# Kernel optimization log

Hardware: AMD Instinct MI355X
Metric: run time of the kernel (lower is better)

## Reference

```python
import jax, jax.numpy as jnp
import numpy as np

DIM = 768
HEADS = 12
HD = DIM // HEADS  # 64
EPS = 1e-5


def _ln(t, g, b):
    # LayerNorm over last axis (head_dim), torch eps=1e-5, biased variance
    mu = jnp.mean(t, axis=-1, keepdims=True)
    var = jnp.mean(jnp.square(t - mu), axis=-1, keepdims=True)
    return (t - mu) * jax.lax.rsqrt(var + EPS) * g + b


def _get_qkv(t, W, bias, gq, bq, gk, bk):
    bs, n, c = t.shape
    qkv = t @ W.T + bias                      # [bs, n, 3c]
    q, k, v = jnp.split(qkv, 3, axis=-1)
    def heads(u):
        return u.reshape(bs, n, HEADS, HD).transpose(0, 2, 1, 3)  # [bs,H,n,hd]
    q, k, v = heads(q), heads(k), heads(v)
    return _ln(q, gq, bq), _ln(k, gk, bk), v


def setup_inputs() -> dict:
    key = jax.random.key(0)
    ks = jax.random.split(key, 12)
    s_in = 1.0 / np.sqrt(DIM)
    d = {
        "x": jax.random.normal(ks[0], (4, 1024, DIM), jnp.float32),
        "y": jax.random.normal(ks[1], (4, 1024, DIM), jnp.float32),
        "Wqkv_x": jax.random.uniform(ks[2], (3 * DIM, DIM), jnp.float32, -s_in, s_in),
        "bqkv_x": jnp.zeros((3 * DIM,), jnp.float32),
        "Wqkv_y": jax.random.uniform(ks[3], (3 * DIM, DIM), jnp.float32, -s_in, s_in),
        "bqkv_y": jnp.zeros((3 * DIM,), jnp.float32),
        "Wproj_x": jax.random.uniform(ks[4], (DIM, DIM), jnp.float32, -s_in, s_in),
        "bproj_x": jnp.zeros((DIM,), jnp.float32),
        "Wproj_y": jax.random.uniform(ks[5], (DIM, DIM), jnp.float32, -s_in, s_in),
        "bproj_y": jnp.zeros((DIM,), jnp.float32),
        "gq_x": jnp.ones((HD,), jnp.float32), "bq_x": jnp.zeros((HD,), jnp.float32),
        "gk_x": jnp.ones((HD,), jnp.float32), "bk_x": jnp.zeros((HD,), jnp.float32),
        "gq_y": jnp.ones((HD,), jnp.float32), "bq_y": jnp.zeros((HD,), jnp.float32),
        "gk_y": jnp.ones((HD,), jnp.float32), "bk_y": jnp.zeros((HD,), jnp.float32),
    }
    return d


def reference(x, y, Wqkv_x, bqkv_x, Wqkv_y, bqkv_y, Wproj_x, bproj_x,
              Wproj_y, bproj_y, gq_x, bq_x, gk_x, bk_x, gq_y, bq_y, gk_y, bk_y):
    bs, n, c = x.shape
    qx, kx, vx = _get_qkv(x, Wqkv_x, bqkv_x, gq_x, bq_x, gk_x, bk_x)
    qy, ky, vy = _get_qkv(y, Wqkv_y, bqkv_y, gq_y, bq_y, gk_y, bk_y)
    q = jnp.concatenate([qx, qy], axis=2)     # [bs,H,n+m,hd]
    k = jnp.concatenate([kx, ky], axis=2)
    v = jnp.concatenate([vx, vy], axis=2)
    score = jnp.einsum("bhqd,bhkd->bhqk", q, k) / np.sqrt(HD)
    attn = jax.nn.softmax(score, axis=-1)
    out = jnp.einsum("bhqk,bhkd->bhqd", attn, v)  # [bs,H,n+m,hd]
    out = out.transpose(0, 2, 1, 3).reshape(bs, -1, c)
    ox, oy = out[:, :n, :], out[:, n:, :]
    return ox @ Wproj_x.T + bproj_x, oy @ Wproj_y.T + bproj_y
```

## Files before the change

### kernel.cpp

```cpp
#include <hip/hip_runtime.h>
#include <stdint.h>

typedef unsigned int u32;
typedef __attribute__((ext_vector_type(8))) __bf16 bf16x8;
typedef __attribute__((ext_vector_type(8))) short s16x8;
typedef __attribute__((ext_vector_type(4))) short s16x4;
typedef __attribute__((ext_vector_type(4))) float f32x4;


__device__ __forceinline__ short f2bf(float f) {
    __bf16 h = (__bf16)f;
    return __builtin_bit_cast(short, h);
}

__device__ __forceinline__ bf16x8 asbf(s16x8 v) {
    return __builtin_bit_cast(bf16x8, v);
}

__device__ __forceinline__ void gl_lds16(const void* g, void* l) {
    __builtin_amdgcn_global_load_lds((__attribute__((address_space(1))) u32*)g,
                                     (__attribute__((address_space(3))) u32*)l,
                                     16, 0, 0);
}



__global__ __launch_bounds__(256) void pack_tiles(
    const float* __restrict__ x,  short* __restrict__ xP,
    const float* __restrict__ y,  short* __restrict__ yP,
    const float* __restrict__ wqx, short* __restrict__ wqxP,
    const float* __restrict__ wqy, short* __restrict__ wqyP,
    const float* __restrict__ wpx, short* __restrict__ wpxP,
    const float* __restrict__ wpy, short* __restrict__ wpyP)
{
    const int tid  = threadIdx.x;
    const int w    = tid >> 6, lane = tid & 63;
    const int lam  = lane & 15, quad = lane >> 4;

    int t = blockIdx.x;
    const float* src; short* dst;
    if (t < 384)                 { src = x;   dst = xP; }
    else if ((t -= 384) < 384)   { src = y;   dst = yP; }
    else if ((t -= 384) < 216)   { src = wqx; dst = wqxP; }
    else if ((t -= 216) < 216)   { src = wqy; dst = wqyP; }
    else if ((t -= 216) < 72)    { src = wpx; dst = wpxP; }
    else                         { t -= 72;  src = wpy; dst = wpyP; }

    const int kb = t % 12, rb = t / 12;
    const int m0 = rb * 128, k0 = kb * 64;
    short* dtile = dst + (size_t)t * 8192;

    #pragma unroll
    for (int u = 0; u < 2; u++) {
        const int ig = w * 2 + u;
        #pragma unroll
        for (int c = 0; c < 2; c++) {
            const float* sp = src + (size_t)(m0 + ig * 16 + lam) * 768 + k0 + c * 32 + quad * 8;
            f32x4 a = *(const f32x4*)sp;
            f32x4 b = *(const f32x4*)(sp + 4);
            s16x8 o;
            o[0] = f2bf(a.x); o[1] = f2bf(a.y); o[2] = f2bf(a.z); o[3] = f2bf(a.w);
            o[4] = f2bf(b.x); o[5] = f2bf(b.y); o[6] = f2bf(b.z); o[7] = f2bf(b.w);
            *(s16x8*)(dtile + (c * 8 + ig) * 512 + lane * 8) = o;
        }
    }
}


__device__ __forceinline__ void stage_qkv(
    const short* __restrict__ At, const short* __restrict__ Wt,
    short* __restrict__ dA, short* __restrict__ dB, int w, int lane)
{
    #pragma unroll
    for (int c = 0; c < 2; c++)
        #pragma unroll
        for (int h = 0; h < 2; h++) {
            const int ch = c * 8 + w + h * 4;
            gl_lds16(At + ch * 512 + lane * 8, dA + ch * 512);
            gl_lds16(Wt + ch * 512 + lane * 8, dB + ch * 512);
        }
}

__global__ __launch_bounds__(256, 2) void qkv_gemm(
    const short* __restrict__ AxP, const short* __restrict__ AyP,
    const short* __restrict__ WxP, const short* __restrict__ WyP,
    const float* __restrict__ biasx, const float* __restrict__ biasy,
    const float* __restrict__ gqx, const float* __restrict__ bqx,
    const float* __restrict__ gkx, const float* __restrict__ bkx,
    const float* __restrict__ gqy, const float* __restrict__ bqy,
    const float* __restrict__ gky, const float* __restrict__ bky,
    short* __restrict__ Q, short* __restrict__ KP, short* __restrict__ VP)
{
    __shared__ union {
        struct { short a[8192]; short b[8192]; } st;
        short e[4][5120];
    } uL;
    const int tid  = threadIdx.x;
    const int w    = tid >> 6, lane = tid & 63;
    const int lam  = lane & 15, quad = lane >> 4;
    const int strm = blockIdx.z;
    const int mblk = blockIdx.x;
    const int nblk = blockIdx.y;
    const short* AP   = strm ? AyP : AxP;
    const short* WP   = strm ? WyP : WxP;
    const float* bias = strm ? biasy : biasx;
    const int m0 = mblk * 128;
    const int n0 = nblk * 128;
    const int wm = w >> 1, wn = w & 1;

    const f32x4 fzero = {0.f, 0.f, 0.f, 0.f};
    f32x4 acc[4][4];
    #pragma unroll
    for (int i = 0; i < 4; i++)
        #pragma unroll
        for (int t = 0; t < 4; t++) acc[i][t] = fzero;

    for (int kb = 0; kb < 12; ++kb) {
        __syncthreads();
        stage_qkv(AP + (size_t)(mblk * 12 + kb) * 8192,
                  WP + (size_t)(nblk * 12 + kb) * 8192,
                  uL.st.a, uL.st.b, w, lane);
        __syncthreads();
        s16x8 af[2][4], bfr[2][4];
        #pragma unroll
        for (int c = 0; c < 2; c++)
            #pragma unroll
            for (int i = 0; i < 4; i++)
                af[c][i] = *(const s16x8*)(uL.st.a + ((c * 8 + wm * 4 + i) * 64 + lane) * 8);
        #pragma unroll
        for (int c = 0; c < 2; c++)
            #pragma unroll
            for (int t = 0; t < 4; t++)
                bfr[c][t] = *(const s16x8*)(uL.st.b + ((c * 8 + wn * 4 + t) * 64 + lane) * 8);
        #pragma unroll
        for (int c = 0; c < 2; c++)
            #pragma unroll
            for (int i = 0; i < 4; i++)
                #pragma unroll
                for (int t = 0; t < 4; t++)
                    acc[i][t] = __builtin_amdgcn_mfma_f32_16x16x32_bf16(
                        asbf(af[c][i]), asbf(bfr[c][t]), acc[i][t], 0, 0, 0);
    }
    __syncthreads();

    const int nb     = n0 + wn * 64;
    const int region = nb / 768;
    const int head   = (nb % 768) / 64;
    const int mg0    = m0 + wm * 64;
    const int b_     = mg0 >> 10;
    const int sg0    = (mg0 & 1023) + strm * 1024;
    short* myE = uL.e[w];

    float bv[4];
    #pragma unroll
    for (int t = 0; t < 4; t++) bv[t] = bias[nb + t * 16 + lam];
    float gv[4], bb[4];
    if (region < 2) {
        const float* gp = (region == 0) ? (strm ? gqy : gqx) : (strm ? gky : gkx);
        const float* bp = (region == 0) ? (strm ? bqy : bqx) : (strm ? bky : bkx);
        #pragma unroll
        for (int t = 0; t < 4; t++) { gv[t] = gp[t * 16 + lam]; bb[t] = bp[t * 16 + lam]; }
    }

    #pragma unroll
    for (int i = 0; i < 4; i++) {
        #pragma unroll
        for (int reg = 0; reg < 4; reg++) {
            const int lr = i * 16 + quad * 4 + reg;
            float v0 = acc[i][0][reg] + bv[0];
            float v1 = acc[i][1][reg] + bv[1];
            float v2 = acc[i][2][reg] + bv[2];
            float v3 = acc[i][3][reg] + bv[3];
            if (region < 2) {
                float s = v0 + v1 + v2 + v3;
                s += __shfl_xor(s, 1); s += __shfl_xor(s, 2);
                s += __shfl_xor(s, 4); s += __shfl_xor(s, 8);
                const float mean = s * (1.f / 64.f);
                const float c0 = v0 - mean, c1 = v1 - mean, c2 = v2 - mean, c3 = v3 - mean;
                float q2 = c0 * c0 + c1 * c1 + c2 * c2 + c3 * c3;
                q2 += __shfl_xor(q2, 1); q2 += __shfl_xor(q2, 2);
                q2 += __shfl_xor(q2, 4); q2 += __shfl_xor(q2, 8);
                const float rs = rsqrtf(q2 * (1.f / 64.f) + 1e-5f);
                v0 = c0 * rs * gv[0] + bb[0];
                v1 = c1 * rs * gv[1] + bb[1];
                v2 = c2 * rs * gv[2] + bb[2];
                v3 = c3 * rs * gv[3] + bb[3];
                myE[lr * 80 + 0 * 16 + lam] = f2bf(v0);
                myE[lr * 80 + 1 * 16 + lam] = f2bf(v1);
                myE[lr * 80 + 2 * 16 + lam] = f2bf(v2);
                myE[lr * 80 + 3 * 16 + lam] = f2bf(v3);
            } else {
                myE[(0 * 16 + lam) * 80 + lr] = f2bf(v0);
                myE[(1 * 16 + lam) * 80 + lr] = f2bf(v1);
                myE[(2 * 16 + lam) * 80 + lr] = f2bf(v2);
                myE[(3 * 16 + lam) * 80 + lr] = f2bf(v3);
            }
        }
    }

    if (region == 0) {
        const int l8 = lane >> 3, c8 = (lane & 7) * 8;
        short* dstp = Q + ((size_t)(b_ * 12 + head) * 2048 + sg0) * 64;
        #pragma unroll
        for (int j = 0; j < 8; j++) {
            const int rr = j * 8 + l8;
            *(s16x8*)(dstp + (size_t)rr * 64 + c8) = *(const s16x8*)(myE + rr * 80 + c8);
        }
    } else {
        short* dstp = (region == 1 ? KP : VP) +
                      ((size_t)(b_ * 12 + head) * 32 + (sg0 >> 6)) * 4096;
        #pragma unroll
        for (int c = 0; c < 2; c++)
            #pragma unroll
            for (int ig = 0; ig < 4; ig++) {
                s16x8 vv = *(const s16x8*)(myE + (ig * 16 + lam) * 80 + c * 32 + quad * 8);
                *(s16x8*)(dstp + (c * 4 + ig) * 512 + lane * 8) = vv;
            }
    }
}


__global__ __launch_bounds__(256, 3) void attn(
    const short* __restrict__ Q, const short* __restrict__ KP,
    const short* __restrict__ VP, short* __restrict__ OP)
{
    __shared__ union {
        struct { short k[2][4096]; short v[2][4096]; } kv;
        short o[4][2560];
    } uL;
    __shared__ __align__(16) short lP[4][1088];
    const int tid  = threadIdx.x;
    const int w    = tid >> 6, lane = tid & 63;
    const int lam  = lane & 15, quad = lane >> 4;
    const int bh   = blockIdx.x;
    const int q0   = blockIdx.y * 128 + w * 32;
    const short* Qb  = Q  + (size_t)bh * 2048 * 64;
    const short* KPb = KP + (size_t)bh * 32 * 4096;
    const short* VPb = VP + (size_t)bh * 32 * 4096;
    short* myP = lP[w];

    s16x8 aq[2][2];
    #pragma unroll
    for (int qf = 0; qf < 2; qf++)
        #pragma unroll
        for (int c = 0; c < 2; c++)
            aq[qf][c] = *(const s16x8*)(Qb + (size_t)(q0 + qf * 16 + lam) * 64 + c * 32 + quad * 8);

    const f32x4 fzero = {0.f, 0.f, 0.f, 0.f};
    f32x4 o[2][4];
    float lsum[2][4];
    #pragma unroll
    for (int qf = 0; qf < 2; qf++) {
        #pragma unroll
        for (int t = 0; t < 4; t++) o[qf][t] = fzero;
        #pragma unroll
        for (int r = 0; r < 4; r++) lsum[qf][r] = 0.f;
    }

    #define STAGE(st_, bi_)                                                             \
        do {                                                                            \
            const short* kt = KPb + (size_t)(st_) * 4096;                               \
            const short* vt = VPb + (size_t)(st_) * 4096;                               \
            _Pragma("unroll")                                                           \
            for (int u_ = 0; u_ < 2; u_++) {                                            \
                const int ch_ = w * 2 + u_;                                             \
                gl_lds16(kt + ch_ * 512 + lane * 8, &uL.kv.k[bi_][ch_ * 512]);          \
                gl_lds16(vt + ch_ * 512 + lane * 8, &uL.kv.v[bi_][ch_ * 512]);          \
            }                                                                           \
        } while (0)

    STAGE(0, 0);
    __syncthreads();

    const float c1 = 0.18033688011112042f;
    int bi = 0;
    for (int it = 0; it < 32; ++it) {
        if (it + 1 < 32) STAGE(it + 1, bi ^ 1);

        const short* cK = uL.kv.k[bi];
        const short* cV = uL.kv.v[bi];
        #pragma unroll
        for (int qf = 0; qf < 2; qf++) {
            f32x4 sc[4];
            #pragma unroll
            for (int t = 0; t < 4; t++) sc[t] = fzero;
            #pragma unroll
            for (int t = 0; t < 4; t++) {
                s16x8 k0 = *(const s16x8*)(cK + ((0 * 4 + t) * 512 + lane * 8));
                s16x8 k1 = *(const s16x8*)(cK + ((1 * 4 + t) * 512 + lane * 8));
                sc[t] = __builtin_amdgcn_mfma_f32_16x16x32_bf16(asbf(aq[qf][0]), asbf(k0), sc[t], 0, 0, 0);
                sc[t] = __builtin_amdgcn_mfma_f32_16x16x32_bf16(asbf(aq[qf][1]), asbf(k1), sc[t], 0, 0, 0);
            }
            #pragma unroll
            for (int t = 0; t < 4; t++) {
                const int g = t * 2 + (lam >> 3);
                #pragma unroll
                for (int r = 0; r < 4; r++) {
                    const float p = __builtin_amdgcn_exp2f(__builtin_fmaf(sc[t][r], c1, -30.f));
                    lsum[qf][r] += p;
                    myP[(g * 17 + quad * 4 + r) * 8 + (lam & 7)] = f2bf(p);
                }
            }
            s16x8 ap0 = *(const s16x8*)(myP + (quad * 17 + lam) * 8);
            s16x8 ap1 = *(const s16x8*)(myP + ((4 + quad) * 17 + lam) * 8);
            #pragma unroll
            for (int t = 0; t < 4; t++) {
                s16x8 v0 = *(const s16x8*)(cV + ((0 * 4 + t) * 512 + lane * 8));
                s16x8 v1 = *(const s16x8*)(cV + ((1 * 4 + t) * 512 + lane * 8));
                o[qf][t] = __builtin_amdgcn_mfma_f32_16x16x32_bf16(asbf(ap0), asbf(v0), o[qf][t], 0, 0, 0);
                o[qf][t] = __builtin_amdgcn_mfma_f32_16x16x32_bf16(asbf(ap1), asbf(v1), o[qf][t], 0, 0, 0);
            }
        }
        __syncthreads();
        bi ^= 1;
    }
    #undef STAGE

    short* myO = uL.o[w];
    #pragma unroll
    for (int qf = 0; qf < 2; qf++) {
        #pragma unroll
        for (int r = 0; r < 4; r++) {
            float l = lsum[qf][r];
            l += __shfl_xor(l, 1); l += __shfl_xor(l, 2);
            l += __shfl_xor(l, 4); l += __shfl_xor(l, 8);
            const float inv = 1.0f / l;
            const int row = qf * 16 + quad * 4 + r;
            #pragma unroll
            for (int t = 0; t < 4; t++)
                myO[row * 80 + t * 16 + lam] = f2bf(o[qf][t][r] * inv);
        }
    }

    const int b_ = bh / 12, h_ = bh % 12;
    const int strm = q0 >> 10;
    const int s    = q0 & 1023;
    const int sb   = s >> 6;
    short* dstp = OP + (((size_t)((strm * 4 + b_) * 16 + sb)) * 12 + h_) * 4096;
    const int igb = (s & 63) >> 4;
    #pragma unroll
    for (int u = 0; u < 2; u++) {
        const int ig = igb + u;
        #pragma unroll
        for (int c = 0; c < 2; c++) {
            s16x8 vv = *(const s16x8*)(myO + (u * 16 + lam) * 80 + c * 32 + quad * 8);
            *(s16x8*)(dstp + (c * 4 + ig) * 512 + lane * 8) = vv;
        }
    }
}


__device__ __forceinline__ void stage_proj(
    const short* __restrict__ Ot, const short* __restrict__ Wt,
    short* __restrict__ dA, short* __restrict__ dB, int w, int lane)
{
    #pragma unroll
    for (int u = 0; u < 2; u++) {
        const int ch = w * 2 + u;
        gl_lds16(Ot + ch * 512 + lane * 8, dA + ch * 512);
    }
    #pragma unroll
    for (int c = 0; c < 2; c++)
        #pragma unroll
        for (int h = 0; h < 2; h++) {
            const int ch = c * 8 + w + h * 4;
            gl_lds16(Wt + ch * 512 + lane * 8, dB + ch * 512);
        }
}

__global__ __launch_bounds__(256, 3) void proj_gemm(
    const short* __restrict__ OP,
    const short* __restrict__ WpxP, const short* __restrict__ WpyP,
    const float* __restrict__ bpx, const float* __restrict__ bpy,
    float* __restrict__ out)
{
    __shared__ __align__(16) short lA[2][4096];
    __shared__ __align__(16) short lB[2][8192];
    const int tid  = threadIdx.x;
    const int w    = tid >> 6, lane = tid & 63;
    const int lam  = lane & 15, quad = lane >> 4;
    const int strm = blockIdx.z;
    const short* WP   = strm ? WpyP : WpxP;
    const float* bias = strm ? bpy : bpx;
    const int m0 = blockIdx.x * 64;
    const int n0 = blockIdx.y * 128;
    const int wm = w >> 1, wn = w & 1;

    const int b_ = m0 >> 10, sb = (m0 & 1023) >> 6;
    const size_t tA0 = ((size_t)((strm * 4 + b_) * 16 + sb)) * 12;
    const size_t tB0 = (size_t)blockIdx.y * 12;

    const f32x4 fzero = {0.f, 0.f, 0.f, 0.f};
    f32x4 acc[2][4];
    #pragma unroll
    for (int i = 0; i < 2; i++)
        #pragma unroll
        for (int t = 0; t < 4; t++) acc[i][t] = fzero;

    stage_proj(OP + tA0 * 4096, WP + tB0 * 8192, lA[0], lB[0], w, lane);
    __syncthreads();

    int bi = 0;
    for (int kb = 0; kb < 12; ++kb) {
        if (kb + 1 < 12)
            stage_proj(OP + (tA0 + kb + 1) * 4096, WP + (tB0 + kb + 1) * 8192,
                       lA[bi ^ 1], lB[bi ^ 1], w, lane);

        const short* cA = lA[bi];
        const short* cB = lB[bi];
        s16x8 af[2][2], bfr[2][4];
        #pragma unroll
        for (int c = 0; c < 2; c++)
            #pragma unroll
            for (int i = 0; i < 2; i++)
                af[c][i] = *(const s16x8*)(cA + ((c * 4 + wm * 2 + i) * 64 + lane) * 8);
        #pragma unroll
        for (int c = 0; c < 2; c++)
            #pragma unroll
            for (int t = 0; t < 4; t++)
                bfr[c][t] = *(const s16x8*)(cB + ((c * 8 + wn * 4 + t) * 64 + lane) * 8);
        #pragma unroll
        for (int c = 0; c < 2; c++)
            #pragma unroll
            for (int i = 0; i < 2; i++)
                #pragma unroll
                for (int t = 0; t < 4; t++)
                    acc[i][t] = __builtin_amdgcn_mfma_f32_16x16x32_bf16(
                        asbf(af[c][i]), asbf(bfr[c][t]), acc[i][t], 0, 0, 0);

        __syncthreads();
        bi ^= 1;
    }

    const int nb = n0 + wn * 64;
    float bv[4];
    #pragma unroll
    for (int t = 0; t < 4; t++) bv[t] = bias[nb + t * 16 + lam];
    #pragma unroll
    for (int i = 0; i < 2; i++) {
        #pragma unroll
        for (int reg = 0; reg < 4; reg++) {
            const int mg = m0 + wm * 32 + i * 16 + quad * 4 + reg;
            float* dst = out + (size_t)strm * 3145728 + (size_t)mg * 768 + nb;
            #pragma unroll
            for (int t = 0; t < 4; t++) dst[t * 16 + lam] = acc[i][t][reg] + bv[t];
        }
    }
}


#define WS_XP  0
#define WS_YP  6291456
#define WS_WQX 12582912
#define WS_WQY 16121856
#define WS_WPX 19660800
#define WS_WPY 20840448
#define WS_Q   22020096
#define WS_KP  34603008
#define WS_VP  47185920
#define WS_OP  59768832

extern "C" void kernel_launch(void* const* d_in, const int* in_sizes, int n_in,
                              void* d_out, int out_size, void* d_ws, size_t ws_size,
                              hipStream_t stream) {
    (void)in_sizes; (void)n_in; (void)out_size; (void)ws_size;
    const float* x       = (const float*)d_in[0];
    const float* y       = (const float*)d_in[1];
    const float* Wqkv_x  = (const float*)d_in[2];
    const float* bqkv_x  = (const float*)d_in[3];
    const float* Wqkv_y  = (const float*)d_in[4];
    const float* bqkv_y  = (const float*)d_in[5];
    const float* Wproj_x = (const float*)d_in[6];
    const float* bproj_x = (const float*)d_in[7];
    const float* Wproj_y = (const float*)d_in[8];
    const float* bproj_y = (const float*)d_in[9];
    const float* gq_x = (const float*)d_in[10];
    const float* bq_x = (const float*)d_in[11];
    const float* gk_x = (const float*)d_in[12];
    const float* bk_x = (const float*)d_in[13];
    const float* gq_y = (const float*)d_in[14];
    const float* bq_y = (const float*)d_in[15];
    const float* gk_y = (const float*)d_in[16];
    const float* bk_y = (const float*)d_in[17];

    char* ws = (char*)d_ws;
    short* xP   = (short*)(ws + WS_XP);
    short* yP   = (short*)(ws + WS_YP);
    short* wqxP = (short*)(ws + WS_WQX);
    short* wqyP = (short*)(ws + WS_WQY);
    short* wpxP = (short*)(ws + WS_WPX);
    short* wpyP = (short*)(ws + WS_WPY);
    short* Qb   = (short*)(ws + WS_Q);
    short* KPb  = (short*)(ws + WS_KP);
    short* VPb  = (short*)(ws + WS_VP);
    short* OPb  = (short*)(ws + WS_OP);

    pack_tiles<<<1344, 256, 0, stream>>>(x, xP, y, yP, Wqkv_x, wqxP,
                                         Wqkv_y, wqyP, Wproj_x, wpxP, Wproj_y, wpyP);

    dim3 g1(32, 18, 2);
    qkv_gemm<<<g1, 256, 0, stream>>>(xP, yP, wqxP, wqyP, bqkv_x, bqkv_y,
                                     gq_x, bq_x, gk_x, bk_x,
                                     gq_y, bq_y, gk_y, bk_y,
                                     Qb, KPb, VPb);

    dim3 g2(48, 16);
    attn<<<g2, 256, 0, stream>>>(Qb, KPb, VPb, OPb);

    dim3 g3(64, 6, 2);
    proj_gemm<<<g3, 256, 0, stream>>>(OPb, wpxP, wpyP, bproj_x, bproj_y, (float*)d_out);
}
```

Baseline: 251.7 us.

## Load K/V fragments straight from global into registers, dropping LDS staging

Removes the double-buffered global-to-LDS staging of K and V tiles and the per-iteration block barrier. Each wave now reads its K/V MFMA operands directly from global memory into registers and batches the score and PV MFMAs across both query fragments. The launch-bounds occupancy hint drops from 3 to 2 blocks per CU, and the LDS output buffer is merged into the P scratch array. This trades barrier and LDS traffic for four times the per-block global/L2 reads, since every wave fetches the same tile. It also has no explicit prefetch, so global latency may be exposed on each iteration.

```diff
diff --git a/kernel.cpp b/kernel.cpp
--- a/kernel.cpp
+++ b/kernel.cpp
@@ -220,15 +220,11 @@
 }
 
 
-__global__ __launch_bounds__(256, 3) void attn(
+__global__ __launch_bounds__(256, 2) void attn(
     const short* __restrict__ Q, const short* __restrict__ KP,
     const short* __restrict__ VP, short* __restrict__ OP)
 {
-    __shared__ union {
-        struct { short k[2][4096]; short v[2][4096]; } kv;
-        short o[4][2560];
-    } uL;
-    __shared__ __align__(16) short lP[4][1088];
+    __shared__ __align__(16) short lP[4][2560];
     const int tid  = threadIdx.x;
     const int w    = tid >> 6, lane = tid & 63;
     const int lam  = lane & 15, quad = lane >> 4;
@@ -257,66 +253,69 @@
         for (int r = 0; r < 4; r++) lsum[qf][r] = 0.f;
     }
 
-    #define STAGE(st_, bi_)                                                             \
-        do {                                                                            \
-            const short* kt = KPb + (size_t)(st_) * 4096;                               \
-            const short* vt = VPb + (size_t)(st_) * 4096;                               \
-            _Pragma("unroll")                                                           \
-            for (int u_ = 0; u_ < 2; u_++) {                                            \
-                const int ch_ = w * 2 + u_;                                             \
-                gl_lds16(kt + ch_ * 512 + lane * 8, &uL.kv.k[bi_][ch_ * 512]);          \
-                gl_lds16(vt + ch_ * 512 + lane * 8, &uL.kv.v[bi_][ch_ * 512]);          \
-            }                                                                           \
-        } while (0)
-
-    STAGE(0, 0);
-    __syncthreads();
-
     const float c1 = 0.18033688011112042f;
-    int bi = 0;
+
     for (int it = 0; it < 32; ++it) {
-        if (it + 1 < 32) STAGE(it + 1, bi ^ 1);
-
-        const short* cK = uL.kv.k[bi];
-        const short* cV = uL.kv.v[bi];
+        const short* kt = KPb + (size_t)it * 4096;
+        const short* vt = VPb + (size_t)it * 4096;
+
+        s16x8 kf[4][2];
+        #pragma unroll
+        for (int t = 0; t < 4; t++) {
+            kf[t][0] = *(const s16x8*)(kt + (0 * 4 + t) * 512 + lane * 8);
+            kf[t][1] = *(const s16x8*)(kt + (1 * 4 + t) * 512 + lane * 8);
+        }
+        s16x8 vf[4][2];
+        #pragma unroll
+        for (int t = 0; t < 4; t++) {
+            vf[t][0] = *(const s16x8*)(vt + (0 * 4 + t) * 512 + lane * 8);
+            vf[t][1] = *(const s16x8*)(vt + (1 * 4 + t) * 512 + lane * 8);
+        }
+
+        f32x4 sc[2][4];
+        #pragma unroll
+        for (int qf = 0; qf < 2; qf++)
+            #pragma unroll
+            for (int t = 0; t < 4; t++) sc[qf][t] = fzero;
+        #pragma unroll
+        for (int t = 0; t < 4; t++)
+            #pragma unroll
+            for (int qf = 0; qf < 2; qf++) {
+                sc[qf][t] = __builtin_amdgcn_mfma_f32_16x16x32_bf16(
+                    asbf(aq[qf][0]), asbf(kf[t][0]), sc[qf][t], 0, 0, 0);
+                sc[qf][t] = __builtin_amdgcn_mfma_f32_16x16x32_bf16(
+                    asbf(aq[qf][1]), asbf(kf[t][1]), sc[qf][t], 0, 0, 0);
+            }
+
+        s16x8 ap[2][2];
         #pragma unroll
         for (int qf = 0; qf < 2; qf++) {
-            f32x4 sc[4];
-            #pragma unroll
-            for (int t = 0; t < 4; t++) sc[t] = fzero;
-            #pragma unroll
-            for (int t = 0; t < 4; t++) {
-                s16x8 k0 = *(const s16x8*)(cK + ((0 * 4 + t) * 512 + lane * 8));
-                s16x8 k1 = *(const s16x8*)(cK + ((1 * 4 + t) * 512 + lane * 8));
-                sc[t] = __builtin_amdgcn_mfma_f32_16x16x32_bf16(asbf(aq[qf][0]), asbf(k0), sc[t], 0, 0, 0);
-                sc[t] = __builtin_amdgcn_mfma_f32_16x16x32_bf16(asbf(aq[qf][1]), asbf(k1), sc[t], 0, 0, 0);
-            }
             #pragma unroll
             for (int t = 0; t < 4; t++) {
                 const int g = t * 2 + (lam >> 3);
                 #pragma unroll
                 for (int r = 0; r < 4; r++) {
-                    const float p = __builtin_amdgcn_exp2f(__builtin_fmaf(sc[t][r], c1, -30.f));
+                    const float p = __builtin_amdgcn_exp2f(__builtin_fmaf(sc[qf][t][r], c1, -30.f));
                     lsum[qf][r] += p;
                     myP[(g * 17 + quad * 4 + r) * 8 + (lam & 7)] = f2bf(p);
                 }
             }
-            s16x8 ap0 = *(const s16x8*)(myP + (quad * 17 + lam) * 8);
-            s16x8 ap1 = *(const s16x8*)(myP + ((4 + quad) * 17 + lam) * 8);
-            #pragma unroll
-            for (int t = 0; t < 4; t++) {
-                s16x8 v0 = *(const s16x8*)(cV + ((0 * 4 + t) * 512 + lane * 8));
-                s16x8 v1 = *(const s16x8*)(cV + ((1 * 4 + t) * 512 + lane * 8));
-                o[qf][t] = __builtin_amdgcn_mfma_f32_16x16x32_bf16(asbf(ap0), asbf(v0), o[qf][t], 0, 0, 0);
-                o[qf][t] = __builtin_amdgcn_mfma_f32_16x16x32_bf16(asbf(ap1), asbf(v1), o[qf][t], 0, 0, 0);
+            ap[qf][0] = *(const s16x8*)(myP + (quad * 17 + lam) * 8);
+            ap[qf][1] = *(const s16x8*)(myP + ((4 + quad) * 17 + lam) * 8);
+        }
+
+        #pragma unroll
+        for (int t = 0; t < 4; t++)
+            #pragma unroll
+            for (int qf = 0; qf < 2; qf++) {
+                o[qf][t] = __builtin_amdgcn_mfma_f32_16x16x32_bf16(
+                    asbf(ap[qf][0]), asbf(vf[t][0]), o[qf][t], 0, 0, 0);
+                o[qf][t] = __builtin_amdgcn_mfma_f32_16x16x32_bf16(
+                    asbf(ap[qf][1]), asbf(vf[t][1]), o[qf][t], 0, 0, 0);
             }
-        }
-        __syncthreads();
-        bi ^= 1;
-    }
-    #undef STAGE
-
-    short* myO = uL.o[w];
+    }
+
+    short* myO = lP[w];
     #pragma unroll
     for (int qf = 0; qf < 2; qf++) {
         #pragma unroll
```

Result: faster. 238.5 us (-5.2%).

## Load K/V fragments directly into registers and fold softmax scale into Q LayerNorm

Applied to the files above, without the earlier changes.

The attention kernel drops its LDS double-buffering of K/V tiles and the per-iteration __syncthreads. Each wave now loads the pre-packed MFMA fragments straight from global memory into registers, with K prefetched one step ahead using ping-pong register arrays. The softmax scale is folded into the Q LayerNorm gamma/beta in the QKV epilogue, and the -30 offset goes in as the MFMA accumulator's initial value, which removes an FMA per score. The cost is redundant global and L2 traffic, since all four waves reload the same K/V tiles. Register pressure also rises, which may hurt occupancy under launch_bounds(256,3).

```diff
diff --git a/kernel.cpp b/kernel.cpp
--- a/kernel.cpp
+++ b/kernel.cpp
@@ -15,6 +15,10 @@
 
 __device__ __forceinline__ bf16x8 asbf(s16x8 v) {
     return __builtin_bit_cast(bf16x8, v);
+}
+
+__device__ __forceinline__ f32x4 mfma32(s16x8 a, s16x8 b, f32x4 c) {
+    return __builtin_amdgcn_mfma_f32_16x16x32_bf16(asbf(a), asbf(b), c, 0, 0, 0);
 }
 
 __device__ __forceinline__ void gl_lds16(const void* g, void* l) {
@@ -138,8 +142,7 @@
             for (int i = 0; i < 4; i++)
                 #pragma unroll
                 for (int t = 0; t < 4; t++)
-                    acc[i][t] = __builtin_amdgcn_mfma_f32_16x16x32_bf16(
-                        asbf(af[c][i]), asbf(bfr[c][t]), acc[i][t], 0, 0, 0);
+                    acc[i][t] = mfma32(af[c][i], bfr[c][t], acc[i][t]);
     }
     __syncthreads();
 
@@ -158,8 +161,9 @@
     if (region < 2) {
         const float* gp = (region == 0) ? (strm ? gqy : gqx) : (strm ? gky : gkx);
         const float* bp = (region == 0) ? (strm ? bqy : bqx) : (strm ? bky : bkx);
-        #pragma unroll
-        for (int t = 0; t < 4; t++) { gv[t] = gp[t * 16 + lam]; bb[t] = bp[t * 16 + lam]; }
+        const float qs  = (region == 0) ? 0.18033688011112042f : 1.0f;
+        #pragma unroll
+        for (int t = 0; t < 4; t++) { gv[t] = gp[t * 16 + lam] * qs; bb[t] = bp[t * 16 + lam] * qs; }
     }
 
     #pragma unroll
@@ -224,11 +228,7 @@
     const short* __restrict__ Q, const short* __restrict__ KP,
     const short* __restrict__ VP, short* __restrict__ OP)
 {
-    __shared__ union {
-        struct { short k[2][4096]; short v[2][4096]; } kv;
-        short o[4][2560];
-    } uL;
-    __shared__ __align__(16) short lP[4][1088];
+    __shared__ __align__(16) short lP[4][2560];
     const int tid  = threadIdx.x;
     const int w    = tid >> 6, lane = tid & 63;
     const int lam  = lane & 15, quad = lane >> 4;
@@ -247,6 +247,7 @@
             aq[qf][c] = *(const s16x8*)(Qb + (size_t)(q0 + qf * 16 + lam) * 64 + c * 32 + quad * 8);
 
     const f32x4 fzero = {0.f, 0.f, 0.f, 0.f};
+    const f32x4 minit = {-30.f, -30.f, -30.f, -30.f};
     f32x4 o[2][4];
     float lsum[2][4];
     #pragma unroll
@@ -257,66 +258,67 @@
         for (int r = 0; r < 4; r++) lsum[qf][r] = 0.f;
     }
 
-    #define STAGE(st_, bi_)                                                             \
-        do {                                                                            \
-            const short* kt = KPb + (size_t)(st_) * 4096;                               \
-            const short* vt = VPb + (size_t)(st_) * 4096;                               \
+    s16x8 kfA[4][2], kfB[4][2];
+    #pragma unroll
+    for (int t = 0; t < 4; t++) {
+        kfA[t][0] = *(const s16x8*)(KPb + (0 * 4 + t) * 512 + lane * 8);
+        kfA[t][1] = *(const s16x8*)(KPb + (1 * 4 + t) * 512 + lane * 8);
+    }
+
+    #define ATTN_STEP(KCUR, KNXT, IT)                                                   \
+        {                                                                               \
+            const short* vt = VPb + (size_t)(IT) * 4096;                                \
+            s16x8 vf[4][2];                                                             \
             _Pragma("unroll")                                                           \
-            for (int u_ = 0; u_ < 2; u_++) {                                            \
-                const int ch_ = w * 2 + u_;                                             \
-                gl_lds16(kt + ch_ * 512 + lane * 8, &uL.kv.k[bi_][ch_ * 512]);          \
-                gl_lds16(vt + ch_ * 512 + lane * 8, &uL.kv.v[bi_][ch_ * 512]);          \
+            for (int t = 0; t < 4; t++) {                                               \
+                vf[t][0] = *(const s16x8*)(vt + (0 * 4 + t) * 512 + lane * 8);          \
+                vf[t][1] = *(const s16x8*)(vt + (1 * 4 + t) * 512 + lane * 8);          \
             }                                                                           \
-        } while (0)
-
-    STAGE(0, 0);
-    __syncthreads();
-
-    const float c1 = 0.18033688011112042f;
-    int bi = 0;
-    for (int it = 0; it < 32; ++it) {
-        if (it + 1 < 32) STAGE(it + 1, bi ^ 1);
-
-        const short* cK = uL.kv.k[bi];
-        const short* cV = uL.kv.v[bi];
-        #pragma unroll
-        for (int qf = 0; qf < 2; qf++) {
-            f32x4 sc[4];
-            #pragma unroll
-            for (int t = 0; t < 4; t++) sc[t] = fzero;
-            #pragma unroll
-            for (int t = 0; t < 4; t++) {
-                s16x8 k0 = *(const s16x8*)(cK + ((0 * 4 + t) * 512 + lane * 8));
-                s16x8 k1 = *(const s16x8*)(cK + ((1 * 4 + t) * 512 + lane * 8));
-                sc[t] = __builtin_amdgcn_mfma_f32_16x16x32_bf16(asbf(aq[qf][0]), asbf(k0), sc[t], 0, 0, 0);
-                sc[t] = __builtin_amdgcn_mfma_f32_16x16x32_bf16(asbf(aq[qf][1]), asbf(k1), sc[t], 0, 0, 0);
-            }
-            #pragma unroll
-            for (int t = 0; t < 4; t++) {
-                const int g = t * 2 + (lam >> 3);
-                #pragma unroll
-                for (int r = 0; r < 4; r++) {
-                    const float p = __builtin_amdgcn_exp2f(__builtin_fmaf(sc[t][r], c1, -30.f));
-                    lsum[qf][r] += p;
-                    myP[(g * 17 + quad * 4 + r) * 8 + (lam & 7)] = f2bf(p);
-                }
-            }
-            s16x8 ap0 = *(const s16x8*)(myP + (quad * 17 + lam) * 8);
-            s16x8 ap1 = *(const s16x8*)(myP + ((4 + quad) * 17 + lam) * 8);
-            #pragma unroll
-            for (int t = 0; t < 4; t++) {
-                s16x8 v0 = *(const s16x8*)(cV + ((0 * 4 + t) * 512 + lane * 8));
-                s16x8 v1 = *(const s16x8*)(cV + ((1 * 4 + t) * 512 + lane * 8));
-                o[qf][t] = __builtin_amdgcn_mfma_f32_16x16x32_bf16(asbf(ap0), asbf(v0), o[qf][t], 0, 0, 0);
-                o[qf][t] = __builtin_amdgcn_mfma_f32_16x16x32_bf16(asbf(ap1), asbf(v1), o[qf][t], 0, 0, 0);
-            }
-        }
-        __syncthreads();
-        bi ^= 1;
-    }
-    #undef STAGE
-
-    short* myO = uL.o[w];
+            if ((IT) + 1 < 32) {                                                        \
+                const short* ktn = KPb + (size_t)((IT) + 1) * 4096;                     \
+                _Pragma("unroll")                                                       \
+                for (int t = 0; t < 4; t++) {                                           \
+                    KNXT[t][0] = *(const s16x8*)(ktn + (0 * 4 + t) * 512 + lane * 8);   \
+                    KNXT[t][1] = *(const s16x8*)(ktn + (1 * 4 + t) * 512 + lane * 8);   \
+                }                                                                       \
+            }                                                                           \
+            _Pragma("unroll")                                                           \
+            for (int qf = 0; qf < 2; qf++) {                                            \
+                f32x4 sc[4];                                                            \
+                _Pragma("unroll")                                                       \
+                for (int t = 0; t < 4; t++) sc[t] = minit;                              \
+                _Pragma("unroll")                                                       \
+                for (int t = 0; t < 4; t++) {                                           \
+                    sc[t] = mfma32(aq[qf][0], KCUR[t][0], sc[t]);                       \
+                    sc[t] = mfma32(aq[qf][1], KCUR[t][1], sc[t]);                       \
+                }                                                                       \
+                _Pragma("unroll")                                                       \
+                for (int t = 0; t < 4; t++) {                                           \
+                    const int g = t * 2 + (lam >> 3);                                   \
+                    _Pragma("unroll")                                                   \
+                    for (int r = 0; r < 4; r++) {                                       \
+                        const float p = __builtin_amdgcn_exp2f(sc[t][r]);               \
+                        lsum[qf][r] += p;                                               \
+                        myP[(g * 17 + quad * 4 + r) * 8 + (lam & 7)] = f2bf(p);         \
+                    }                                                                   \
+                }                                                                       \
+                s16x8 ap0 = *(const s16x8*)(myP + (quad * 17 + lam) * 8);               \
+                s16x8 ap1 = *(const s16x8*)(myP + ((4 + quad) * 17 + lam) * 8);         \
+                _Pragma("unroll")                                                       \
+                for (int t = 0; t < 4; t++) {                                           \
+                    o[qf][t] = mfma32(ap0, vf[t][0], o[qf][t]);                         \
+                    o[qf][t] = mfma32(ap1, vf[t][1], o[qf][t]);                         \
+                }                                                                       \
+            }                                                                           \
+        }
+
+    for (int it2 = 0; it2 < 16; ++it2) {
+        ATTN_STEP(kfA, kfB, it2 * 2);
+        ATTN_STEP(kfB, kfA, it2 * 2 + 1);
+    }
+    #undef ATTN_STEP
+
+    short* myO = myP;
     #pragma unroll
     for (int qf = 0; qf < 2; qf++) {
         #pragma unroll
@@ -425,8 +427,7 @@
             for (int i = 0; i < 2; i++)
                 #pragma unroll
                 for (int t = 0; t < 4; t++)
-                    acc[i][t] = __builtin_amdgcn_mfma_f32_16x16x32_bf16(
-                        asbf(af[c][i]), asbf(bfr[c][t]), acc[i][t], 0, 0, 0);
+                    acc[i][t] = mfma32(af[c][i], bfr[c][t], acc[i][t]);
 
         __syncthreads();
         bi ^= 1;
```

New measurement: 296.2 us. 17.7% more time.
